# Optimization experiments

Hardware: AMD Instinct MI355X
Metric: run time of the kernel (lower is better)

## Reference

```python
import jax, jax.numpy as jnp
import numpy as np

# ---- constants matching the torch module / entmax normmax_bisect defaults ----
ALPHA = 5.0                 # normmax alpha (entmax normmax_bisect default)
N_BISECT = 50               # bisection iterations
K_EXP = 1.0 / (ALPHA - 1.0)        # p_i propto (z_i - tau)_+^{1/(alpha-1)}
AK_EXP = ALPHA / (ALPHA - 1.0)     # norm condition: sum (z-tau)_+^{alpha/(alpha-1)} = 1
EPS = 1e-8                  # module epsilon
LN_EPS = 1e-5               # torch LayerNorm default eps

B, N, C, D = 32, 1024, 64, 768


def _bisect_tau(z):
    # z: [..., S]; find tau with f(tau) = sum_i relu(z_i - tau)^AK_EXP - 1 = 0 (f decreasing)
    max_val = jnp.max(z, axis=-1, keepdims=True)
    lo, hi = max_val - 1.0, max_val  # f(lo) >= 0, f(hi) = -1 < 0

    def body(_, carry):
        lo, hi = carry
        tau = 0.5 * (lo + hi)
        f = jnp.sum(jnp.maximum(z - tau, 0.0) ** AK_EXP, axis=-1, keepdims=True) - 1.0
        lo = jnp.where(f >= 0, tau, lo)
        hi = jnp.where(f >= 0, hi, tau)
        return (lo, hi)

    lo, hi = jax.lax.fori_loop(0, N_BISECT, body, (lo, hi))
    return 0.5 * (lo + hi)


def normmax_last(z):
    # normmax over last axis: p = s / sum(s), s = relu(z - tau)^{1/(alpha-1)}, ||s||_alpha = 1
    tau = _bisect_tau(z)
    u = jnp.maximum(z - tau, 0.0)
    u_safe = jnp.where(u > 0, u, 1.0)
    s = jnp.where(u > 0, u_safe ** K_EXP, 0.0)
    return s / jnp.sum(s, axis=-1, keepdims=True)


def layernorm(x, scale, bias):
    mu = jnp.mean(x, axis=-1, keepdims=True)
    var = jnp.mean((x - mu) ** 2, axis=-1, keepdims=True)
    return (x - mu) * jax.lax.rsqrt(var + LN_EPS) * scale + bias


def setup_inputs() -> dict:
    key = jax.random.key(0)
    ks = jax.random.split(key, 10)
    w = lambda k, shp: (jax.random.normal(k, shp, dtype=jnp.float32) * 0.02)
    return {
        "features": jax.random.normal(ks[0], (B, N, D), dtype=jnp.float32),
        "slots_init": jax.random.normal(ks[1], (B, C, D), dtype=jnp.float32),
        "mask": jax.random.randint(ks[2], (B, N), 0, 2, dtype=jnp.int32),
        "ln_f_scale": jnp.ones((D,), jnp.float32),
        "ln_f_bias": jnp.zeros((D,), jnp.float32),
        "ln_s_scale": jnp.ones((D,), jnp.float32),
        "ln_s_bias": jnp.zeros((D,), jnp.float32),
        "Wk": w(ks[3], (D, D)),
        "Wv": w(ks[4], (D, D)),
        "Wq": w(ks[5], (D, D)),
        "W_ih": w(ks[6], (3 * D, D)),
        "W_hh": w(ks[7], (3 * D, D)),
        "b_ih": jnp.zeros((3 * D,), jnp.float32),
        "b_hh": jnp.zeros((3 * D,), jnp.float32),
    }


def reference(features, slots_init, mask, ln_f_scale, ln_f_bias, ln_s_scale, ln_s_bias,
              Wk, Wv, Wq, W_ih, W_hh, b_ih, b_hh):
    f = layernorm(features, ln_f_scale, ln_f_bias)        # [B,N,D]
    k = f @ Wk.T
    v = f @ Wv.T
    b, n, d = v.shape
    c = slots_init.shape[1]
    m = mask[:, None, :] != 0                             # [B,1,N], broadcasts over C

    # num_iterations = 1; straight-through (detach trick) is the identity here.
    slots_prev = slots_init
    s = layernorm(slots_init, ln_s_scale, ln_s_bias)
    q = s @ Wq.T                                          # [B,C,D]
    logits = jnp.einsum('bcd,bnd->bcn', q, k) * (1.0 / np.sqrt(d))
    logits = jnp.where(m, logits, 0.0)                    # masked_fill(mask==0, 0)
    # normmax over the slot axis (dim=1)
    attn = jnp.moveaxis(normmax_last(jnp.moveaxis(logits, 1, -1)), -1, 1)  # [B,C,N]
    attn = jnp.where(m, attn, 0.0)
    attn_wm = attn / (jnp.sum(attn, axis=-1, keepdims=True) + EPS)
    updates = jnp.einsum('bcn,bnd->bcd', attn_wm, v)      # [B,C,D]

    # torch GRUCell: r,z,n gate order
    x = updates.reshape(-1, d)
    h = slots_prev.reshape(-1, d)
    gi = x @ W_ih.T + b_ih
    gh = h @ W_hh.T + b_hh
    ir, iz, in_ = jnp.split(gi, 3, axis=-1)
    hr, hz, hn = jnp.split(gh, 3, axis=-1)
    r = jax.nn.sigmoid(ir + hr)
    zg = jax.nn.sigmoid(iz + hz)
    ng = jnp.tanh(in_ + r * hn)
    h_new = (1.0 - zg) * ng + zg * h
    slots = h_new.reshape(b, c, d)
    return slots, attn
```

## Files before the change

### kernel.cpp

```cpp
#include <hip/hip_runtime.h>
#include <cstdint>
#include <cmath>

#define DEVINL __device__ __forceinline__


using f32x4  = __attribute__((ext_vector_type(4))) float;
using bf16x8 = __attribute__((ext_vector_type(8))) __bf16;
using u16x8  = __attribute__((ext_vector_type(8))) unsigned short;
using u16x4  = __attribute__((ext_vector_type(4))) unsigned short;
using fl4    = __attribute__((ext_vector_type(4))) float;

DEVINL float bf2f(unsigned short h) {
    unsigned int u = ((unsigned int)h) << 16;
    float f; __builtin_memcpy(&f, &u, 4); return f;
}
DEVINL unsigned short f2bf(float f) {
    unsigned int u; __builtin_memcpy(&u, &f, 4);
    u += 0x7FFFu + ((u >> 16) & 1u);
    return (unsigned short)(u >> 16);
}
DEVINL float sqrt_raw(float x) {
    float r; asm("v_sqrt_f32 %0, %1" : "=v"(r) : "v"(x)); return r;
}

DEVINL void gload_lds16(const unsigned short* g, unsigned short* l) {
    __builtin_amdgcn_global_load_lds(
        (__attribute__((address_space(1))) void*)g,
        (__attribute__((address_space(3))) void*)l,
        16, 0, 0);
}

__global__ __launch_bounds__(256)
void mask_scan_zfill(const int* __restrict__ mask, int* __restrict__ idx,
                     int* __restrict__ cnt, int* __restrict__ cpad,
                     float* __restrict__ zp)
{
    if (blockIdx.x < 2048) {
        const int i = blockIdx.x * 256 + threadIdx.x;
        fl4 z = {0.f, 0.f, 0.f, 0.f};
        *(fl4*)(zp + (long)i * 4) = z;
        return;
    }
    constexpr int NB = 1024;
    const int b = (blockIdx.x - 2048) * 4 + (threadIdx.x >> 6);
    const int lane = threadIdx.x & 63;
    if (b >= 32) return;
    const int* mrow = mask + b * NB;
    int loc[16]; int lsum = 0;
#pragma unroll
    for (int i = 0; i < 16; ++i) { loc[i] = mrow[lane * 16 + i] != 0; lsum += loc[i]; }
    int pre = lsum;
#pragma unroll
    for (int o = 1; o < 64; o <<= 1) {
        int t = __shfl_up(pre, o);
        if (lane >= o) pre += t;
    }
    const int total = __shfl(pre, 63);
    pre -= lsum;
    int* ib = idx + b * NB;
    int p = pre;
#pragma unroll
    for (int i = 0; i < 16; ++i) if (loc[i]) ib[p++] = lane * 16 + i;
    if (lane == 0) {
        cnt[b] = total;
        int cp = (total + 63) & ~63;
        cpad[b] = cp < 64 ? 64 : cp;
    }
}

__global__ __launch_bounds__(256)
void tr2_f2b_split(const float* __restrict__ Wq, const float* __restrict__ Wk,
                   unsigned short* __restrict__ WqT_i, unsigned short* __restrict__ WkT_i)
{
    constexpr int S = 768 * 768;
    const int o = blockIdx.x * 256 + threadIdx.x;
    if (o >= 2 * S) return;
    const float* x; unsigned short* y; int i;
    if (o < S) { x = Wq; y = WqT_i; i = o; }
    else       { x = Wk; y = WkT_i; i = o - S; }
    const int e = i / 768, d = i - e * 768;
    const float v = x[d * 768 + e];
    const unsigned short h = f2bf(v);
    y[(long)e * 1536 + d]       = h;
    y[(long)e * 1536 + 768 + d] = f2bf(v - bf2f(h));
}

__global__ __launch_bounds__(256)
void conv2_fused(const float* __restrict__ Wih, const float* __restrict__ Whh,
                 const float* __restrict__ sl,  const float* __restrict__ Wv,
                 unsigned short* __restrict__ Wihb, unsigned short* __restrict__ Whhb,
                 unsigned short* __restrict__ slb,  unsigned short* __restrict__ Wvb)
{
    constexpr int S1 = 3 * 768 * 768;
    constexpr int S2 = S1 + 3 * 768 * 768;
    constexpr int S3 = S2 + 32 * 64 * 768;
    constexpr int S4 = S3 + 768 * 768;
    const int i = (blockIdx.x * 256 + threadIdx.x) * 4;
    if (i >= S4) return;
    const float* src; unsigned short* dst; int off;
    if (i < S1)      { src = Wih; dst = Wihb; off = i; }
    else if (i < S2) { src = Whh; dst = Whhb; off = i - S1; }
    else if (i < S3) { src = sl;  dst = slb;  off = i - S2; }
    else             { src = Wv;  dst = Wvb;  off = i - S3; }
    fl4 v = *(const fl4*)(src + off);
    u16x4 o;
#pragma unroll
    for (int j = 0; j < 4; ++j) o[j] = f2bf(v[j]);
    *(u16x4*)(dst + off) = o;
}

template<int BM, int BN, int WAVES_M, int WAVES_N, int OUTMODE>
__global__ __launch_bounds__(256)
void gemm_bt3(const unsigned short* __restrict__ AB, const unsigned short* __restrict__ BB,
              void* __restrict__ out1, const int* __restrict__ cpad,
              int N, int K, long sA, long sB, long sC, float alpha)
{
    constexpr int BK = 32;
    constexpr int WM = BM / WAVES_M, WN = BN / WAVES_N;
    constexpr int MT = WM / 16, NT = WN / 16;
    __shared__ alignas(16) unsigned short Ash[BM * BK], Asl[BM * BK];
    __shared__ alignas(16) unsigned short Bsh[BN * BK], Bsl[BN * BK];

    const int bz = blockIdx.z;
    const int row0 = blockIdx.y * BM, col0 = blockIdx.x * BN;
    if (cpad && col0 >= cpad[bz]) return;
    AB += (long)bz * sA;
    BB += (long)bz * sB;
    const int tid = threadIdx.x, l = tid & 63, w = tid >> 6;
    const int wm = w / WAVES_N, wn = w % WAVES_N;
    const int fr = l & 15, fq = l >> 4;

    f32x4 acc[MT][NT] = {};
    constexpr int ACALLS = (BM * BK) / (256 * 8);
    constexpr int BCALLS = (BN * BK) / (256 * 8);

    for (int kt = 0; kt < K; kt += BK) {
#pragma unroll
        for (int c = 0; c < ACALLS; ++c) {
            const int e = (c * 256 + tid) * 8;
            const long rb = (long)(row0 + (e >> 5)) * (2 * K) + kt + (e & 31);
            gload_lds16(AB + rb, &Ash[e]);
            gload_lds16(AB + rb + K, &Asl[e]);
        }
#pragma unroll
        for (int c = 0; c < BCALLS; ++c) {
            const int e = (c * 256 + tid) * 8;
            const long rb = (long)(col0 + (e >> 5)) * (2 * K) + kt + (e & 31);
            gload_lds16(BB + rb, &Bsh[e]);
            gload_lds16(BB + rb + K, &Bsl[e]);
        }
        __syncthreads();

        bf16x8 afh[MT], afl[MT], bfh[NT], bfl[NT];
#pragma unroll
        for (int m = 0; m < MT; ++m) {
            const int o = (wm * WM + m * 16 + fr) * BK + fq * 8;
            afh[m] = __builtin_bit_cast(bf16x8, *(const u16x8*)&Ash[o]);
            afl[m] = __builtin_bit_cast(bf16x8, *(const u16x8*)&Asl[o]);
        }
#pragma unroll
        for (int n = 0; n < NT; ++n) {
            const int o = (wn * WN + n * 16 + fr) * BK + fq * 8;
            bfh[n] = __builtin_bit_cast(bf16x8, *(const u16x8*)&Bsh[o]);
            bfl[n] = __builtin_bit_cast(bf16x8, *(const u16x8*)&Bsl[o]);
        }
#pragma unroll
        for (int m = 0; m < MT; ++m)
#pragma unroll
            for (int n = 0; n < NT; ++n) {
                acc[m][n] = __builtin_amdgcn_mfma_f32_16x16x32_bf16(afh[m], bfh[n], acc[m][n], 0, 0, 0);
                acc[m][n] = __builtin_amdgcn_mfma_f32_16x16x32_bf16(afh[m], bfl[n], acc[m][n], 0, 0, 0);
                acc[m][n] = __builtin_amdgcn_mfma_f32_16x16x32_bf16(afl[m], bfh[n], acc[m][n], 0, 0, 0);
            }
        __syncthreads();
    }

#pragma unroll
    for (int m = 0; m < MT; ++m) {
        const int gr = row0 + wm * WM + m * 16 + fq * 4;
#pragma unroll
        for (int n = 0; n < NT; ++n) {
            const int gc = col0 + wn * WN + n * 16 + fr;
#pragma unroll
            for (int j = 0; j < 4; ++j) {
                const float v = acc[m][n][j] * alpha;
                if (OUTMODE == 0) {
                    ((float*)out1)[(long)bz * sC + (long)(gr + j) * N + gc] = v;
                } else {
                    unsigned short* ob = (unsigned short*)out1;
                    const long rb = (long)(gr + j) * (2 * N) + gc;
                    const unsigned short h = f2bf(v);
                    ob[rb] = h;
                    ob[rb + N] = f2bf(v - bf2f(h));
                }
            }
        }
    }
}

template<int BM, int BN, int WAVES_M, int WAVES_N, bool OUT_F32>
__global__ __launch_bounds__(256)
void gemm_bt(const unsigned short* __restrict__ A,
             const unsigned short* __restrict__ B,
             void* __restrict__ Cv,
             int N, int K, long sA, long sB, long sC, float alpha)
{
    constexpr int BK = 32;
    constexpr int WM = BM / WAVES_M, WN = BN / WAVES_N;
    constexpr int MT = WM / 16, NT = WN / 16;
    __shared__ alignas(16) unsigned short As[BM * BK];
    __shared__ alignas(16) unsigned short Bs[BN * BK];

    const int bz = blockIdx.z;
    A += (long)bz * sA;
    B += (long)bz * sB;
    const int row0 = blockIdx.y * BM, col0 = blockIdx.x * BN;
    const int tid = threadIdx.x, l = tid & 63, w = tid >> 6;
    const int wm = w / WAVES_N, wn = w % WAVES_N;
    const int fr = l & 15, fq = l >> 4;

    f32x4 acc[MT][NT] = {};
    constexpr int ACALLS = (BM * BK) / (256 * 8);
    constexpr int BCALLS = (BN * BK) / (256 * 8);

    for (int kt = 0; kt < K; kt += BK) {
#pragma unroll
        for (int c = 0; c < ACALLS; ++c) {
            const int e = (c * 256 + tid) * 8;
            gload_lds16(A + (long)(row0 + (e >> 5)) * K + kt + (e & 31), &As[e]);
        }
#pragma unroll
        for (int c = 0; c < BCALLS; ++c) {
            const int e = (c * 256 + tid) * 8;
            gload_lds16(B + (long)(col0 + (e >> 5)) * K + kt + (e & 31), &Bs[e]);
        }
        __syncthreads();

        bf16x8 af[MT], bfr[NT];
#pragma unroll
        for (int m = 0; m < MT; ++m)
            af[m] = __builtin_bit_cast(bf16x8, *(const u16x8*)&As[(wm * WM + m * 16 + fr) * BK + fq * 8]);
#pragma unroll
        for (int n = 0; n < NT; ++n)
            bfr[n] = __builtin_bit_cast(bf16x8, *(const u16x8*)&Bs[(wn * WN + n * 16 + fr) * BK + fq * 8]);
#pragma unroll
        for (int m = 0; m < MT; ++m)
#pragma unroll
            for (int n = 0; n < NT; ++n)
                acc[m][n] = __builtin_amdgcn_mfma_f32_16x16x32_bf16(af[m], bfr[n], acc[m][n], 0, 0, 0);
        __syncthreads();
    }

#pragma unroll
    for (int m = 0; m < MT; ++m) {
        const int gr = row0 + wm * WM + m * 16 + fq * 4;
#pragma unroll
        for (int n = 0; n < NT; ++n) {
            const int gc = col0 + wn * WN + n * 16 + fr;
#pragma unroll
            for (int j = 0; j < 4; ++j) {
                const float v = acc[m][n][j] * alpha;
                if (OUT_F32) ((float*)Cv)[(long)bz * sC + (long)(gr + j) * N + gc] = v;
                else ((unsigned short*)Cv)[(long)bz * sC + (long)(gr + j) * N + gc] = f2bf(v);
            }
        }
    }
}

__global__ __launch_bounds__(256)
void gemm_gru(const unsigned short* __restrict__ updb, const unsigned short* __restrict__ slb,
              const unsigned short* __restrict__ Wihb, const unsigned short* __restrict__ Whhb,
              const float* __restrict__ b_ih, const float* __restrict__ b_hh,
              const float* __restrict__ h, float* __restrict__ out)
{
    constexpr int BK = 32, Kd = 768, Dd = 768;
    __shared__ alignas(16) unsigned short Au[64 * BK], As[64 * BK];
    __shared__ alignas(16) unsigned short Bi[3][64 * BK], Bh[3][64 * BK];

    const int row0 = blockIdx.y * 64, col0 = blockIdx.x * 64;
    const int tid = threadIdx.x, l = tid & 63, w = tid >> 6;
    const int wm = w >> 1, wn = w & 1;
    const int fr = l & 15, fq = l >> 4;

    f32x4 ai[3][2][2] = {}, ah[3][2][2] = {};

    for (int kt = 0; kt < Kd; kt += BK) {
        {
            const int e = tid * 8;
            const long rb = (long)(row0 + (e >> 5)) * Kd + kt + (e & 31);
            gload_lds16(updb + rb, &Au[e]);
            gload_lds16(slb + rb, &As[e]);
#pragma unroll
            for (int g = 0; g < 3; ++g) {
                const long wb = (long)(g * Dd + col0 + (e >> 5)) * Kd + kt + (e & 31);
                gload_lds16(Wihb + wb, &Bi[g][e]);
                gload_lds16(Whhb + wb, &Bh[g][e]);
            }
        }
        __syncthreads();

        bf16x8 au[2], as_[2], bi[3][2], bh[3][2];
#pragma unroll
        for (int m = 0; m < 2; ++m) {
            const int o = (wm * 32 + m * 16 + fr) * BK + fq * 8;
            au[m]  = __builtin_bit_cast(bf16x8, *(const u16x8*)&Au[o]);
            as_[m] = __builtin_bit_cast(bf16x8, *(const u16x8*)&As[o]);
        }
#pragma unroll
        for (int n = 0; n < 2; ++n) {
            const int o = (wn * 32 + n * 16 + fr) * BK + fq * 8;
#pragma unroll
            for (int g = 0; g < 3; ++g) {
                bi[g][n] = __builtin_bit_cast(bf16x8, *(const u16x8*)&Bi[g][o]);
                bh[g][n] = __builtin_bit_cast(bf16x8, *(const u16x8*)&Bh[g][o]);
            }
        }
#pragma unroll
        for (int g = 0; g < 3; ++g)
#pragma unroll
            for (int m = 0; m < 2; ++m)
#pragma unroll
                for (int n = 0; n < 2; ++n) {
                    ai[g][m][n] = __builtin_amdgcn_mfma_f32_16x16x32_bf16(au[m],  bi[g][n], ai[g][m][n], 0, 0, 0);
                    ah[g][m][n] = __builtin_amdgcn_mfma_f32_16x16x32_bf16(as_[m], bh[g][n], ah[g][m][n], 0, 0, 0);
                }
        __syncthreads();
    }

#pragma unroll
    for (int m = 0; m < 2; ++m) {
        const int gr = row0 + wm * 32 + m * 16 + fq * 4;
#pragma unroll
        for (int n = 0; n < 2; ++n) {
            const int gc = col0 + wn * 32 + n * 16 + fr;
            const float bir = b_ih[gc],        bhr = b_hh[gc];
            const float biz = b_ih[Dd + gc],   bhz = b_hh[Dd + gc];
            const float bin = b_ih[2*Dd + gc], bhn = b_hh[2*Dd + gc];
#pragma unroll
            for (int j = 0; j < 4; ++j) {
                const float r  = 1.f / (1.f + expf(-(ai[0][m][n][j] + bir + ah[0][m][n][j] + bhr)));
                const float zg = 1.f / (1.f + expf(-(ai[1][m][n][j] + biz + ah[1][m][n][j] + bhz)));
                const float ng = tanhf(ai[2][m][n][j] + bin + r * (ah[2][m][n][j] + bhn));
                const long idx = (long)(gr + j) * Dd + gc;
                out[idx] = (1.f - zg) * ng + zg * h[idx];
            }
        }
    }
}

template<int BM, int BN, int WAVES_M, int WAVES_N>
__global__ __launch_bounds__(256)
void gemm_nt_rs(const unsigned short* __restrict__ A,
                const unsigned short* __restrict__ Bm,
                unsigned short* __restrict__ C,
                const int* __restrict__ cpad,
                int N, int Kmax, long sA, long sB, long sC)
{
    constexpr int BK = 32;
    constexpr int WM = BM / WAVES_M, WN = BN / WAVES_N;
    constexpr int MT = WM / 16, NT = WN / 16;
    __shared__ alignas(16) unsigned short As[BM * BK];
    __shared__ alignas(16) unsigned short Bs[BN * BK];
    __shared__ float rsums[BM];

    const int bz = blockIdx.z;
    const int Keff = cpad[bz];
    A += (long)bz * sA;
    Bm += (long)bz * sB;
    const int row0 = blockIdx.y * BM, col0 = blockIdx.x * BN;
    const int tid = threadIdx.x, l = tid & 63, w = tid >> 6;
    const int wm = w / WAVES_N, wn = w % WAVES_N;
    const int fr = l & 15, fq = l >> 4;

    f32x4 acc[MT][NT] = {};
    float rsum = 0.f;
    constexpr int ACALLS = (BM * BK) / (256 * 8);
    constexpr int TPR = BN / 8;
    constexpr int RPP = 256 / TPR;
    const int br = tid / TPR, bc8 = (tid % TPR) * 8;

    for (int kt = 0; kt < Keff; kt += BK) {
#pragma unroll
        for (int c = 0; c < ACALLS; ++c) {
            const int e = (c * 256 + tid) * 8;
            gload_lds16(A + (long)(row0 + (e >> 5)) * Kmax + kt + (e & 31), &As[e]);
        }
#pragma unroll
        for (int p = 0; p < BK / RPP; ++p) {
            const int r = p * RPP + br;
            u16x8 vv = *(const u16x8*)(Bm + (long)(kt + r) * (2 * N) + col0 + bc8);
#pragma unroll
            for (int j = 0; j < 8; ++j) Bs[(bc8 + j) * BK + r] = vv[j];
        }
        __syncthreads();

        if (tid < BM) {
#pragma unroll
            for (int kk = 0; kk < BK / 8; ++kk) {
                u16x8 vv = *(const u16x8*)&As[tid * BK + kk * 8];
#pragma unroll
                for (int j = 0; j < 8; ++j) rsum += bf2f(vv[j]);
            }
        }

        bf16x8 af[MT], bfr[NT];
#pragma unroll
        for (int m = 0; m < MT; ++m)
            af[m] = __builtin_bit_cast(bf16x8, *(const u16x8*)&As[(wm * WM + m * 16 + fr) * BK + fq * 8]);
#pragma unroll
        for (int n = 0; n < NT; ++n)
            bfr[n] = __builtin_bit_cast(bf16x8, *(const u16x8*)&Bs[(wn * WN + n * 16 + fr) * BK + fq * 8]);
#pragma unroll
        for (int m = 0; m < MT; ++m)
#pragma unroll
            for (int n = 0; n < NT; ++n)
                acc[m][n] = __builtin_amdgcn_mfma_f32_16x16x32_bf16(af[m], bfr[n], acc[m][n], 0, 0, 0);
        __syncthreads();
    }

    if (tid < BM) rsums[tid] = rsum;
    __syncthreads();

#pragma unroll
    for (int m = 0; m < MT; ++m) {
        const int lr = wm * WM + m * 16 + fq * 4;
        const int gr = row0 + lr;
#pragma unroll
        for (int n = 0; n < NT; ++n) {
            const int gc = col0 + wn * WN + n * 16 + fr;
#pragma unroll
            for (int j = 0; j < 4; ++j) {
                const float inv = 1.f / (rsums[lr + j] + 1e-8f);
                C[(long)bz * sC + (long)(gr + j) * N + gc] = f2bf(acc[m][n][j] * inv);
            }
        }
    }
}

__global__ __launch_bounds__(256)
void ln_fused_c(const float* __restrict__ xf, const float* __restrict__ gf,
                const float* __restrict__ bf,
                unsigned short* __restrict__ fi,
                const float* __restrict__ xs, const float* __restrict__ gs,
                const float* __restrict__ bs,
                unsigned short* __restrict__ si,
                const int* __restrict__ idx, const int* __restrict__ cnt,
                const int* __restrict__ cpad, int nrows_f)
{
    constexpr int D = 768;
    const int lane = threadIdx.x & 63;
    long row = (long)blockIdx.x * 4 + (threadIdx.x >> 6);
    const float *x, *g, *bb_;
    long srow;
    if (row < nrows_f) {
        const int b = (int)(row >> 10), j = (int)(row & 1023);
        if (j >= cpad[b]) return;
        srow = row;
        unsigned short* yr = fi + srow * (2 * D);
        if (j >= cnt[b]) {
            u16x8 z = {};
            unsigned short* p = yr + lane * 24;
            *(u16x8*)p = z; *(u16x8*)(p + 8) = z; *(u16x8*)(p + 16) = z;
            return;
        }
        const int n = idx[(b << 10) + j];
        x = xf + ((long)(b << 10) + n) * D;
        g = gf; bb_ = bf;
    } else {
        srow = row - nrows_f;
        x = xs + srow * D;
        g = gs; bb_ = bs;
    }

    const int eA = lane * 8;
    const int eB = 512 + lane * 8;
    float v[16];
    {
        fl4 a = *(const fl4*)(x + eA);
        fl4 b = *(const fl4*)(x + eA + 4);
#pragma unroll
        for (int j = 0; j < 4; ++j) { v[j] = a[j]; v[4 + j] = b[j]; }
    }
    if (lane < 32) {
        fl4 a = *(const fl4*)(x + eB);
        fl4 b = *(const fl4*)(x + eB + 4);
#pragma unroll
        for (int j = 0; j < 4; ++j) { v[8 + j] = a[j]; v[12 + j] = b[j]; }
    }
    float s = 0.f, s2 = 0.f;
#pragma unroll
    for (int j = 0; j < 8; ++j) { s += v[j]; s2 += v[j] * v[j]; }
    if (lane < 32) {
#pragma unroll
        for (int j = 8; j < 16; ++j) { s += v[j]; s2 += v[j] * v[j]; }
    }
#pragma unroll
    for (int o = 1; o < 64; o <<= 1) { s += __shfl_xor(s, o); s2 += __shfl_xor(s2, o); }
    const float mu  = s / (float)D;
    const float var = s2 / (float)D - mu * mu;
    const float r   = rsqrtf(var + 1e-5f);

    unsigned short* yr = (row < nrows_f ? fi : si) + srow * (2 * D);
    {
        fl4 g0 = *(const fl4*)(g + eA), g1 = *(const fl4*)(g + eA + 4);
        fl4 b0 = *(const fl4*)(bb_ + eA), b1 = *(const fl4*)(bb_ + eA + 4);
        u16x8 oh, ol;
#pragma unroll
        for (int j = 0; j < 8; ++j) {
            const float gg = (j < 4) ? g0[j] : g1[j - 4];
            const float be = (j < 4) ? b0[j] : b1[j - 4];
            const float yv = (v[j] - mu) * r * gg + be;
            oh[j] = f2bf(yv);
            ol[j] = f2bf(yv - bf2f(oh[j]));
        }
        *(u16x8*)(yr + eA) = oh;
        *(u16x8*)(yr + D + eA) = ol;
    }
    if (lane < 32) {
        fl4 g0 = *(const fl4*)(g + eB), g1 = *(const fl4*)(g + eB + 4);
        fl4 b0 = *(const fl4*)(bb_ + eB), b1 = *(const fl4*)(bb_ + eB + 4);
        u16x8 oh, ol;
#pragma unroll
        for (int j = 0; j < 8; ++j) {
            const float gg = (j < 4) ? g0[j] : g1[j - 4];
            const float be = (j < 4) ? b0[j] : b1[j - 4];
            const float yv = (v[8 + j] - mu) * r * gg + be;
            oh[j] = f2bf(yv);
            ol[j] = f2bf(yv - bf2f(oh[j]));
        }
        *(u16x8*)(yr + eB) = oh;
        *(u16x8*)(yr + D + eB) = ol;
    }
}

__global__ __launch_bounds__(256)
void normmax_cols_c(const float* __restrict__ logits,
                    const int* __restrict__ idx, const int* __restrict__ cnt,
                    const int* __restrict__ cpad,
                    float* __restrict__ attn_f32, unsigned short* __restrict__ attn_b16)
{
    constexpr int N = 1024, C = 64;
    const int b = blockIdx.y;
    const int j0 = blockIdx.x * 64;
    if (j0 >= cpad[b]) return;
    const int tid = threadIdx.x, l = tid & 63, w = tid >> 6;
    const int j = j0 + w * 16 + (l & 15);
    const int cb = (l >> 4) * 16;
    const long base = (long)b * C * N + j;
    const bool valid = j < cnt[b];

    float z[16];
#pragma unroll
    for (int i = 0; i < 16; ++i) z[i] = valid ? logits[base + (long)(cb + i) * N] : 0.f;

    float mx = z[0];
#pragma unroll
    for (int i = 1; i < 16; ++i) mx = fmaxf(mx, z[i]);
    mx = fmaxf(mx, __shfl_xor(mx, 16));
    mx = fmaxf(mx, __shfl_xor(mx, 32));

    float lo = mx - 1.f, hi = mx;
    for (int it = 0; it < 34; ++it) {
        const float tau = 0.5f * (lo + hi);
        float f = 0.f;
#pragma unroll
        for (int i = 0; i < 16; ++i) {
            const float u = fmaxf(z[i] - tau, 0.f);
            f += u * sqrt_raw(sqrt_raw(u));
        }
        f += __shfl_xor(f, 16);
        f += __shfl_xor(f, 32);
        if (f >= 1.f) lo = tau; else hi = tau;
    }
    const float tau = 0.5f * (lo + hi);
    float sv[16]; float ss = 0.f;
#pragma unroll
    for (int i = 0; i < 16; ++i) {
        const float u = fmaxf(z[i] - tau, 0.f);
        sv[i] = sqrt_raw(sqrt_raw(u));
        ss += sv[i];
    }
    ss += __shfl_xor(ss, 16);
    ss += __shfl_xor(ss, 32);
    const float inv = 1.f / ss;
    const int n = valid ? idx[(b << 10) + j] : 0;
#pragma unroll
    for (int i = 0; i < 16; ++i) {
        const float a = valid ? sv[i] * inv : 0.f;
        attn_b16[base + (long)(cb + i) * N] = f2bf(a);
        if (valid) attn_f32[(long)b * C * N + (long)(cb + i) * N + n] = a;
    }
}

extern "C" void kernel_launch(void* const* d_in, const int* in_sizes, int n_in,
                              void* d_out, int out_size, void* d_ws, size_t ws_size,
                              hipStream_t stream)
{
    const float* features = (const float*)d_in[0];
    const float* slots    = (const float*)d_in[1];
    const int*   mask     = (const int*)d_in[2];
    const float* lnf_g = (const float*)d_in[3];
    const float* lnf_b = (const float*)d_in[4];
    const float* lns_g = (const float*)d_in[5];
    const float* lns_b = (const float*)d_in[6];
    const float* Wk  = (const float*)d_in[7];
    const float* Wv  = (const float*)d_in[8];
    const float* Wq  = (const float*)d_in[9];
    const float* Wih = (const float*)d_in[10];
    const float* Whh = (const float*)d_in[11];
    const float* bih = (const float*)d_in[12];
    const float* bhh = (const float*)d_in[13];

    constexpr int B = 32, N = 1024, C = 64, D = 768;
    char* ws = (char*)d_ws;
    unsigned short* f_i  = (unsigned short*)(ws + 0);
    unsigned short* Wihb = (unsigned short*)(ws + 37748736);
    unsigned short* Whhb = (unsigned short*)(ws + 41287680);
    unsigned short* Wvb  = (unsigned short*)(ws + 44826624);
    unsigned short* updb = (unsigned short*)(ws + 57671680);
    unsigned short* slb  = (unsigned short*)(ws + 60817408);
    float*          lg     = (float*)(ws + 100663296);
    unsigned short* s_i    = (unsigned short*)(ws + 109051904);
    unsigned short* ab16   = (unsigned short*)(ws + 109051904);
    unsigned short* qk_i   = (unsigned short*)(ws + 115343360);
    unsigned short* Pbf    = (unsigned short*)(ws + 115343360);
    unsigned short* WqT_i  = (unsigned short*)(ws + 121634816);
    unsigned short* WkT_i  = (unsigned short*)(ws + 123994112);
    unsigned short* M_i    = (unsigned short*)(ws + 126353408);
    int*            idx    = (int*)(ws + 128712704);
    int*            cnt    = (int*)(ws + 128843776);
    int*            cpad   = (int*)(ws + 128843904);

    float* out_slots = (float*)d_out;
    float* out_attn  = out_slots + (long)B * C * D;

    mask_scan_zfill<<<2056, 256, 0, stream>>>(mask, idx, cnt, cpad, out_attn);

    tr2_f2b_split<<<(2 * D * D + 255) / 256, 256, 0, stream>>>(Wq, Wk, WqT_i, WkT_i);

    ln_fused_c<<<(B * N + B * C) / 4, 256, 0, stream>>>(
        features, lnf_g, lnf_b, f_i,
        slots, lns_g, lns_b, s_i,
        idx, cnt, cpad, B * N);

    gemm_bt3<64, 64, 2, 2, 1><<<dim3(D / 64, D / 64, 1), 256, 0, stream>>>(
        WkT_i, WqT_i, M_i, nullptr, D, D, 0, 0, 0, 1.f);
    gemm_bt3<64, 64, 2, 2, 1><<<dim3(D / 64, (B * C) / 64, 1), 256, 0, stream>>>(
        s_i, M_i, qk_i, nullptr, D, D, 0, 0, 0, 1.f);
    gemm_bt3<64, 64, 2, 2, 0><<<dim3(N / 64, 1, B), 256, 0, stream>>>(
        qk_i, f_i, lg, cpad,
        N, D, (long)C * 2 * D, (long)N * 2 * D, (long)C * N, 0.03608439182435161f);

    normmax_cols_c<<<dim3(N / 64, B), 256, 0, stream>>>(lg, idx, cnt, cpad, out_attn, ab16);

    gemm_nt_rs<64, 64, 2, 2><<<dim3(D / 64, 1, B), 256, 0, stream>>>(
        ab16, f_i, Pbf, cpad, D, N, (long)C * N, (long)N * 2 * D, (long)C * D);

    {
        constexpr int TOT = 3 * D * D + 3 * D * D + B * C * D + D * D;
        conv2_fused<<<(TOT / 4 + 255) / 256, 256, 0, stream>>>(
            Wih, Whh, slots, Wv, Wihb, Whhb, slb, Wvb);
    }

    gemm_bt<64, 64, 2, 2, false><<<dim3(D / 64, (B * C) / 64, 1), 256, 0, stream>>>(
        Pbf, Wvb, updb, D, D, 0, 0, 0, 1.f);

    gemm_gru<<<dim3(D / 64, (B * C) / 64), 256, 0, stream>>>(
        updb, slb, Wihb, Whhb, bih, bhh, slots, out_slots);
}
```

Baseline: 197.4 us.

## Fuse logits GEMM with normmax bisection and merge preprocessing kernels

The q·k logits GEMM now keeps its 64x64 output tile in shared memory and runs the normmax bisection directly on it. This removes the fp32 logits round trip through global memory and one kernel launch. The mask scan/zero-fill kernel and the Wq/Wk transpose-split kernel are also merged into one launch. In exchange, the fused kernel uses more shared memory per block (an extra 64x65 float tile), which may lower occupancy.

```diff
diff --git a/kernel.cpp b/kernel.cpp
--- a/kernel.cpp
+++ b/kernel.cpp
@@ -32,9 +32,11 @@
 }
 
 __global__ __launch_bounds__(256)
-void mask_scan_zfill(const int* __restrict__ mask, int* __restrict__ idx,
-                     int* __restrict__ cnt, int* __restrict__ cpad,
-                     float* __restrict__ zp)
+void preproc(const int* __restrict__ mask, int* __restrict__ idx,
+             int* __restrict__ cnt, int* __restrict__ cpad,
+             float* __restrict__ zp,
+             const float* __restrict__ Wq, const float* __restrict__ Wk,
+             unsigned short* __restrict__ WqT_i, unsigned short* __restrict__ WkT_i)
 {
     if (blockIdx.x < 2048) {
         const int i = blockIdx.x * 256 + threadIdx.x;
@@ -42,39 +44,36 @@
         *(fl4*)(zp + (long)i * 4) = z;
         return;
     }
-    constexpr int NB = 1024;
-    const int b = (blockIdx.x - 2048) * 4 + (threadIdx.x >> 6);
-    const int lane = threadIdx.x & 63;
-    if (b >= 32) return;
-    const int* mrow = mask + b * NB;
-    int loc[16]; int lsum = 0;
-#pragma unroll
-    for (int i = 0; i < 16; ++i) { loc[i] = mrow[lane * 16 + i] != 0; lsum += loc[i]; }
-    int pre = lsum;
-#pragma unroll
-    for (int o = 1; o < 64; o <<= 1) {
-        int t = __shfl_up(pre, o);
-        if (lane >= o) pre += t;
-    }
-    const int total = __shfl(pre, 63);
-    pre -= lsum;
-    int* ib = idx + b * NB;
-    int p = pre;
-#pragma unroll
-    for (int i = 0; i < 16; ++i) if (loc[i]) ib[p++] = lane * 16 + i;
-    if (lane == 0) {
-        cnt[b] = total;
-        int cp = (total + 63) & ~63;
-        cpad[b] = cp < 64 ? 64 : cp;
-    }
-}
-
-__global__ __launch_bounds__(256)
-void tr2_f2b_split(const float* __restrict__ Wq, const float* __restrict__ Wk,
-                   unsigned short* __restrict__ WqT_i, unsigned short* __restrict__ WkT_i)
-{
+    if (blockIdx.x < 2056) {
+        constexpr int NB = 1024;
+        const int b = (blockIdx.x - 2048) * 4 + (threadIdx.x >> 6);
+        const int lane = threadIdx.x & 63;
+        if (b >= 32) return;
+        const int* mrow = mask + b * NB;
+        int loc[16]; int lsum = 0;
+#pragma unroll
+        for (int i = 0; i < 16; ++i) { loc[i] = mrow[lane * 16 + i] != 0; lsum += loc[i]; }
+        int pre = lsum;
+#pragma unroll
+        for (int o = 1; o < 64; o <<= 1) {
+            int t = __shfl_up(pre, o);
+            if (lane >= o) pre += t;
+        }
+        const int total = __shfl(pre, 63);
+        pre -= lsum;
+        int* ib = idx + b * NB;
+        int p = pre;
+#pragma unroll
+        for (int i = 0; i < 16; ++i) if (loc[i]) ib[p++] = lane * 16 + i;
+        if (lane == 0) {
+            cnt[b] = total;
+            int cp = (total + 63) & ~63;
+            cpad[b] = cp < 64 ? 64 : cp;
+        }
+        return;
+    }
     constexpr int S = 768 * 768;
-    const int o = blockIdx.x * 256 + threadIdx.x;
+    const int o = (blockIdx.x - 2056) * 256 + threadIdx.x;
     if (o >= 2 * S) return;
     const float* x; unsigned short* y; int i;
     if (o < S) { x = Wq; y = WqT_i; i = o; }
@@ -110,11 +109,11 @@
     *(u16x4*)(dst + off) = o;
 }
 
-template<int BM, int BN, int WAVES_M, int WAVES_N, int OUTMODE>
+template<int BM, int BN, int WAVES_M, int WAVES_N>
 __global__ __launch_bounds__(256)
-void gemm_bt3(const unsigned short* __restrict__ AB, const unsigned short* __restrict__ BB,
-              void* __restrict__ out1, const int* __restrict__ cpad,
-              int N, int K, long sA, long sB, long sC, float alpha)
+void gemm_bt3s(const unsigned short* __restrict__ AB, const unsigned short* __restrict__ BB,
+               unsigned short* __restrict__ out1,
+               int N, int K, long sA, long sB, float alpha)
 {
     constexpr int BK = 32;
     constexpr int WM = BM / WAVES_M, WN = BN / WAVES_N;
@@ -124,7 +123,6 @@
 
     const int bz = blockIdx.z;
     const int row0 = blockIdx.y * BM, col0 = blockIdx.x * BN;
-    if (cpad && col0 >= cpad[bz]) return;
     AB += (long)bz * sA;
     BB += (long)bz * sB;
     const int tid = threadIdx.x, l = tid & 63, w = tid >> 6;
@@ -185,17 +183,134 @@
 #pragma unroll
             for (int j = 0; j < 4; ++j) {
                 const float v = acc[m][n][j] * alpha;
-                if (OUTMODE == 0) {
-                    ((float*)out1)[(long)bz * sC + (long)(gr + j) * N + gc] = v;
-                } else {
-                    unsigned short* ob = (unsigned short*)out1;
-                    const long rb = (long)(gr + j) * (2 * N) + gc;
-                    const unsigned short h = f2bf(v);
-                    ob[rb] = h;
-                    ob[rb + N] = f2bf(v - bf2f(h));
-                }
-            }
-        }
+                const long rb = (long)(gr + j) * (2 * N) + gc;
+                const unsigned short h = f2bf(v);
+                out1[rb] = h;
+                out1[rb + N] = f2bf(v - bf2f(h));
+            }
+        }
+    }
+}
+
+__global__ __launch_bounds__(256)
+void logits_normmax(const unsigned short* __restrict__ qk_i,
+                    const unsigned short* __restrict__ f_i,
+                    const int* __restrict__ idx, const int* __restrict__ cnt,
+                    const int* __restrict__ cpad,
+                    float* __restrict__ attn_f32, unsigned short* __restrict__ attn_b16)
+{
+    constexpr int BK = 32, K = 768, C = 64, N = 1024;
+    constexpr float alpha = 0.03608439182435161f;
+    const int b = blockIdx.y;
+    const int col0 = blockIdx.x * 64;
+    if (col0 >= cpad[b]) return;
+
+    __shared__ alignas(16) unsigned short Ash[64 * BK], Asl[64 * BK];
+    __shared__ alignas(16) unsigned short Bsh[64 * BK], Bsl[64 * BK];
+    __shared__ float lgS[64][65];
+
+    const unsigned short* AB = qk_i + (long)b * C * 2 * K;
+    const unsigned short* BB = f_i + (long)b * N * 2 * K;
+    const int tid = threadIdx.x, l = tid & 63, w = tid >> 6;
+    const int wm = w >> 1, wn = w & 1;
+    const int fr = l & 15, fq = l >> 4;
+
+    f32x4 acc[2][2] = {};
+
+    for (int kt = 0; kt < K; kt += BK) {
+        {
+            const int e = tid * 8;
+            const long ra = (long)(e >> 5) * (2 * K) + kt + (e & 31);
+            gload_lds16(AB + ra, &Ash[e]);
+            gload_lds16(AB + ra + K, &Asl[e]);
+            const long rb = (long)(col0 + (e >> 5)) * (2 * K) + kt + (e & 31);
+            gload_lds16(BB + rb, &Bsh[e]);
+            gload_lds16(BB + rb + K, &Bsl[e]);
+        }
+        __syncthreads();
+
+        bf16x8 afh[2], afl[2], bfh[2], bfl[2];
+#pragma unroll
+        for (int m = 0; m < 2; ++m) {
+            const int o = (wm * 32 + m * 16 + fr) * BK + fq * 8;
+            afh[m] = __builtin_bit_cast(bf16x8, *(const u16x8*)&Ash[o]);
+            afl[m] = __builtin_bit_cast(bf16x8, *(const u16x8*)&Asl[o]);
+        }
+#pragma unroll
+        for (int n = 0; n < 2; ++n) {
+            const int o = (wn * 32 + n * 16 + fr) * BK + fq * 8;
+            bfh[n] = __builtin_bit_cast(bf16x8, *(const u16x8*)&Bsh[o]);
+            bfl[n] = __builtin_bit_cast(bf16x8, *(const u16x8*)&Bsl[o]);
+        }
+#pragma unroll
+        for (int m = 0; m < 2; ++m)
+#pragma unroll
+            for (int n = 0; n < 2; ++n) {
+                acc[m][n] = __builtin_amdgcn_mfma_f32_16x16x32_bf16(afh[m], bfh[n], acc[m][n], 0, 0, 0);
+                acc[m][n] = __builtin_amdgcn_mfma_f32_16x16x32_bf16(afh[m], bfl[n], acc[m][n], 0, 0, 0);
+                acc[m][n] = __builtin_amdgcn_mfma_f32_16x16x32_bf16(afl[m], bfh[n], acc[m][n], 0, 0, 0);
+            }
+        __syncthreads();
+    }
+
+#pragma unroll
+    for (int m = 0; m < 2; ++m) {
+        const int lr = wm * 32 + m * 16 + fq * 4;
+#pragma unroll
+        for (int n = 0; n < 2; ++n) {
+            const int lc = wn * 32 + n * 16 + fr;
+#pragma unroll
+            for (int j = 0; j < 4; ++j) lgS[lr + j][lc] = acc[m][n][j] * alpha;
+        }
+    }
+    __syncthreads();
+
+    const int jl = w * 16 + (l & 15);
+    const int cb = (l >> 4) * 16;
+    const int j = col0 + jl;
+    const bool valid = j < cnt[b];
+
+    float z[16];
+#pragma unroll
+    for (int i = 0; i < 16; ++i) z[i] = valid ? lgS[cb + i][jl] : 0.f;
+
+    float mx = z[0];
+#pragma unroll
+    for (int i = 1; i < 16; ++i) mx = fmaxf(mx, z[i]);
+    mx = fmaxf(mx, __shfl_xor(mx, 16));
+    mx = fmaxf(mx, __shfl_xor(mx, 32));
+
+    float lo = mx - 1.f, hi = mx;
+    for (int it = 0; it < 34; ++it) {
+        const float tau = 0.5f * (lo + hi);
+        float f = 0.f;
+#pragma unroll
+        for (int i = 0; i < 16; ++i) {
+            const float u = fmaxf(z[i] - tau, 0.f);
+            f += u * sqrt_raw(sqrt_raw(u));
+        }
+        f += __shfl_xor(f, 16);
+        f += __shfl_xor(f, 32);
+        if (f >= 1.f) lo = tau; else hi = tau;
+    }
+    const float tau = 0.5f * (lo + hi);
+    float sv[16]; float ss = 0.f;
+#pragma unroll
+    for (int i = 0; i < 16; ++i) {
+        const float u = fmaxf(z[i] - tau, 0.f);
+        sv[i] = sqrt_raw(sqrt_raw(u));
+        ss += sv[i];
+    }
+    ss += __shfl_xor(ss, 16);
+    ss += __shfl_xor(ss, 32);
+    const float inv = 1.f / ss;
+    const long base = (long)b * C * N + j;
+    const int n_orig = valid ? idx[(b << 10) + j] : 0;
+#pragma unroll
+    for (int i = 0; i < 16; ++i) {
+        const float a = valid ? sv[i] * inv : 0.f;
+        attn_b16[base + (long)(cb + i) * N] = f2bf(a);
+        if (valid) attn_f32[(long)b * C * N + (long)(cb + i) * N + n_orig] = a;
     }
 }
 
@@ -534,65 +649,6 @@
     }
 }
 
-__global__ __launch_bounds__(256)
-void normmax_cols_c(const float* __restrict__ logits,
-                    const int* __restrict__ idx, const int* __restrict__ cnt,
-                    const int* __restrict__ cpad,
-                    float* __restrict__ attn_f32, unsigned short* __restrict__ attn_b16)
-{
-    constexpr int N = 1024, C = 64;
-    const int b = blockIdx.y;
-    const int j0 = blockIdx.x * 64;
-    if (j0 >= cpad[b]) return;
-    const int tid = threadIdx.x, l = tid & 63, w = tid >> 6;
-    const int j = j0 + w * 16 + (l & 15);
-    const int cb = (l >> 4) * 16;
-    const long base = (long)b * C * N + j;
-    const bool valid = j < cnt[b];
-
-    float z[16];
-#pragma unroll
-    for (int i = 0; i < 16; ++i) z[i] = valid ? logits[base + (long)(cb + i) * N] : 0.f;
-
-    float mx = z[0];
-#pragma unroll
-    for (int i = 1; i < 16; ++i) mx = fmaxf(mx, z[i]);
-    mx = fmaxf(mx, __shfl_xor(mx, 16));
-    mx = fmaxf(mx, __shfl_xor(mx, 32));
-
-    float lo = mx - 1.f, hi = mx;
-    for (int it = 0; it < 34; ++it) {
-        const float tau = 0.5f * (lo + hi);
-        float f = 0.f;
-#pragma unroll
-        for (int i = 0; i < 16; ++i) {
-            const float u = fmaxf(z[i] - tau, 0.f);
-            f += u * sqrt_raw(sqrt_raw(u));
-        }
-        f += __shfl_xor(f, 16);
-        f += __shfl_xor(f, 32);
-        if (f >= 1.f) lo = tau; else hi = tau;
-    }
-    const float tau = 0.5f * (lo + hi);
-    float sv[16]; float ss = 0.f;
-#pragma unroll
-    for (int i = 0; i < 16; ++i) {
-        const float u = fmaxf(z[i] - tau, 0.f);
-        sv[i] = sqrt_raw(sqrt_raw(u));
-        ss += sv[i];
-    }
-    ss += __shfl_xor(ss, 16);
-    ss += __shfl_xor(ss, 32);
-    const float inv = 1.f / ss;
-    const int n = valid ? idx[(b << 10) + j] : 0;
-#pragma unroll
-    for (int i = 0; i < 16; ++i) {
-        const float a = valid ? sv[i] * inv : 0.f;
-        attn_b16[base + (long)(cb + i) * N] = f2bf(a);
-        if (valid) attn_f32[(long)b * C * N + (long)(cb + i) * N + n] = a;
-    }
-}
-
 extern "C" void kernel_launch(void* const* d_in, const int* in_sizes, int n_in,
                               void* d_out, int out_size, void* d_ws, size_t ws_size,
                               hipStream_t stream)
@@ -620,7 +676,6 @@
     unsigned short* Wvb  = (unsigned short*)(ws + 44826624);
     unsigned short* updb = (unsigned short*)(ws + 57671680);
     unsigned short* slb  = (unsigned short*)(ws + 60817408);
-    float*          lg     = (float*)(ws + 100663296);
     unsigned short* s_i    = (unsigned short*)(ws + 109051904);
     unsigned short* ab16   = (unsigned short*)(ws + 109051904);
     unsigned short* qk_i   = (unsigned short*)(ws + 115343360);
@@ -635,24 +690,21 @@
     float* out_slots = (float*)d_out;
     float* out_attn  = out_slots + (long)B * C * D;
 
-    mask_scan_zfill<<<2056, 256, 0, stream>>>(mask, idx, cnt, cpad, out_attn);
-
-    tr2_f2b_split<<<(2 * D * D + 255) / 256, 256, 0, stream>>>(Wq, Wk, WqT_i, WkT_i);
+    preproc<<<2056 + (2 * D * D + 255) / 256, 256, 0, stream>>>(
+        mask, idx, cnt, cpad, out_attn, Wq, Wk, WqT_i, WkT_i);
 
     ln_fused_c<<<(B * N + B * C) / 4, 256, 0, stream>>>(
         features, lnf_g, lnf_b, f_i,
         slots, lns_g, lns_b, s_i,
         idx, cnt, cpad, B * N);
 
-    gemm_bt3<64, 64, 2, 2, 1><<<dim3(D / 64, D / 64, 1), 256, 0, stream>>>(
-        WkT_i, WqT_i, M_i, nullptr, D, D, 0, 0, 0, 1.f);
-    gemm_bt3<64, 64, 2, 2, 1><<<dim3(D / 64, (B * C) / 64, 1), 256, 0, stream>>>(
-        s_i, M_i, qk_i, nullptr, D, D, 0, 0, 0, 1.f);
-    gemm_bt3<64, 64, 2, 2, 0><<<dim3(N / 64, 1, B), 256, 0, stream>>>(
-        qk_i, f_i, lg, cpad,
-        N, D, (long)C * 2 * D, (long)N * 2 * D, (long)C * N, 0.03608439182435161f);
-
-    normmax_cols_c<<<dim3(N / 64, B), 256, 0, stream>>>(lg, idx, cnt, cpad, out_attn, ab16);
+    gemm_bt3s<64, 64, 2, 2><<<dim3(D / 64, D / 64, 1), 256, 0, stream>>>(
+        WkT_i, WqT_i, M_i, D, D, 0, 0, 1.f);
+    gemm_bt3s<64, 64, 2, 2><<<dim3(D / 64, (B * C) / 64, 1), 256, 0, stream>>>(
+        s_i, M_i, qk_i, D, D, 0, 0, 1.f);
+
+    logits_normmax<<<dim3(N / 64, B), 256, 0, stream>>>(
+        qk_i, f_i, idx, cnt, cpad, out_attn, ab16);
 
     gemm_nt_rs<64, 64, 2, 2><<<dim3(D / 64, 1, B), 256, 0, stream>>>(
         ab16, f_i, Pbf, cpad, D, N, (long)C * N, (long)N * 2 * D, (long)C * D);
```

Result: faster. 187.8 us (-4.9%).
